# Optimization experiments

Measured on AMD Instinct MI355X. Metric: run time of the kernel, lower is better.

The kernel has to match this reference:

```python
import jax, jax.numpy as jnp
import numpy as np

VEC_DIM = 64
RANK = 2


def setup_inputs() -> dict:
    key = jax.random.key(0)
    kg, km, kp = jax.random.split(key, 3)
    grid = jax.random.normal(kg, (193, 193, VEC_DIM), dtype=jnp.float32)
    # nn.init.uniform_(M.weight, -0.5, 0.5)
    M_weight = jax.random.uniform(km, (VEC_DIM, VEC_DIM), minval=-0.5, maxval=0.5, dtype=jnp.float32)
    # nn.init.uniform_(P, -0.1, 0.1)
    P = jax.random.uniform(kp, (VEC_DIM, VEC_DIM), minval=-0.1, maxval=0.1, dtype=jnp.float32)
    return {"grid": grid, "M_weight": M_weight, "P": P}


def reference(grid, M_weight, P):
    H, W, m = grid.shape
    # periods1[i,j] = periods2[i,j] = i*m + j + 2
    periods = (jnp.arange(m, dtype=jnp.float32)[:, None] * m
               + jnp.arange(m, dtype=jnp.float32)[None, :] + 2.0)  # [m, m]

    # ---- window extraction: linear mode (step=1), rank_mode='drop', rank_op='avg' ----
    nH = H - RANK + 1
    nW = W - RANK + 1
    win_sum = jax.lax.reduce_window(grid, 0.0, jax.lax.add,
                                    (RANK, RANK, 1), (1, 1, 1), 'VALID')  # [nH, nW, m]
    x_win = (win_sum / float(RANK * RANK)).reshape(nH * nW, m)  # [B, m]

    # ---- map through M (nn.Linear, no bias): y = x @ W^T ----
    x = x_win @ M_weight.T  # [B, m]

    # ---- phi_table gather: phi[k1,k2] = cos(2*pi*k1/periods) * cos(2*pi*k2/periods) ----
    two_pi = jnp.float32(2.0 * np.pi)
    k1s = jnp.arange(nH, dtype=jnp.float32)
    k2s = jnp.arange(nW, dtype=jnp.float32)
    cos1 = jnp.cos(two_pi * k1s[:, None, None] / periods)  # [nH, m, m]
    cos2 = jnp.cos(two_pi * k2s[:, None, None] / periods)  # [nW, m, m]
    phi = (cos1[:, None, :, :] * cos2[None, :, :, :]).reshape(nH * nW, m, m)  # [B, m, m]

    # ---- Nk = einsum('bj,ij,bij->bi', x, P, phi) ----
    Nk = jnp.einsum('bj,ij,bij->bi', x, P, phi)  # [B, m]
    return Nk
```

## Files before the change

kernel.cpp:

```cpp
#include <hip/hip_runtime.h>
#include <math.h>

#define NH 192
#define NW 192
#define Wt 193
#define TG 24
#define NTILE (TG*TG)
#define TILE_SZ 4096
#define NMAIN 768
#define CHUNK 48

__device__ __forceinline__ float cos_revr(float num, float rcpden) {
    float rev = num * rcpden;
    rev = __builtin_amdgcn_fractf(rev);
    return __builtin_amdgcn_cosf(rev);
}

__global__ __launch_bounds__(256) void k_prep(const float* __restrict__ grid,
                                              const float* __restrict__ Mw,
                                              float* __restrict__ xt) {
    __shared__ float Ms[64 * 64];
    __shared__ float win[64 * 68];
    int bb = blockIdx.x;
    int t = threadIdx.x;
    int k1g = bb % TG, k2g = bb / TG;

    #pragma unroll
    for (int r = 0; r < 4; ++r) {
        int e = r * 256 + t;
        ((float4*)Ms)[e] = ((const float4*)Mw)[e];
    }

    {
        int c = t & 63, pq = t >> 6;
        const float* gb = grid + ((size_t)(k1g * 8) * Wt + k2g * 8) * 64;
        #pragma unroll
        for (int r = 0; r < 16; ++r) {
            int p = pq * 16 + r;
            int l1 = p >> 3, l2 = p & 7;
            const float* g0 = gb + ((size_t)l1 * Wt + l2) * 64;
            float s = g0[c] + g0[64 + c] + g0[Wt * 64 + c] + g0[Wt * 64 + 64 + c];
            win[p * 68 + c] = 0.25f * s;
        }
    }
    __syncthreads();

    int p = t & 63, jq = t >> 6;
    float4 wv[16];
    #pragma unroll
    for (int q = 0; q < 16; ++q) wv[q] = *(const float4*)&win[p * 68 + 4 * q];

    float* xb = xt + (size_t)(k1g * TG + k2g) * TILE_SZ;
    #pragma unroll
    for (int r = 0; r < 16; ++r) {
        int j = jq * 16 + r;
        float acc = 0.f;
        #pragma unroll
        for (int q = 0; q < 16; ++q) {
            float4 mv = *(const float4*)&Ms[j * 64 + 4 * q];
            acc += wv[q].x * mv.x + wv[q].y * mv.y + wv[q].z * mv.z + wv[q].w * mv.w;
        }
        xb[(size_t)j * 64 + p] = acc;
    }
}

__global__ __launch_bounds__(256, 3) void k_main(const float* __restrict__ xt,
                                                 const float* __restrict__ P,
                                                 float* __restrict__ out) {
    __shared__ float xls[CHUNK * 68];
    __shared__ float pp[4096];
    int bx = blockIdx.x;
    int k1 = bx >> 2;
    int c  = bx & 3;
    int k2s = c * CHUNK;
    int t = threadIdx.x;
    int lane = t & 63;
    int w = __builtin_amdgcn_readfirstlane(t >> 6);
    int jb = w * 16;

    {
        const float4* P4 = (const float4*)P;
        #pragma unroll
        for (int s = 0; s < 4; ++s) {
            int e = s * 256 + t;
            float4 v = P4[e];
            int i = e >> 4, j0 = (e & 15) * 4;
            pp[(j0 + 0) * 64 + i] = v.x;
            pp[(j0 + 1) * 64 + i] = v.y;
            pp[(j0 + 2) * 64 + i] = v.z;
            pp[(j0 + 3) * 64 + i] = v.w;
        }
    }
    {
        int prow = k1 & 7;
        const float4* xt4 = (const float4*)xt
                          + (size_t)((k1 >> 3) * TG + c * 6) * (TILE_SZ / 4);
        #pragma unroll
        for (int s = 0; s < 3; ++s) {
            int f = s * 256 + t;
            int j = f / 12, u = f - 12 * j;
            int tc = u >> 1, h = u & 1;
            float4 v = xt4[tc * 1024 + j * 16 + prow * 2 + h];
            int k2l = tc * 8 + h * 4;
            xls[(k2l + 0) * 68 + j] = v.x;
            xls[(k2l + 1) * 68 + j] = v.y;
            xls[(k2l + 2) * 68 + j] = v.z;
            xls[(k2l + 3) * 68 + j] = v.w;
        }
    }
    __syncthreads();

    float A[16], c1v[16], ce[16], co[16];
    #pragma unroll
    for (int jl = 0; jl < 16; ++jl) {
        float T  = (float)(lane * 64 + jb + jl + 2);
        float rT = __builtin_amdgcn_rcpf(T);
        A[jl]   = 2.0f * cos_revr(1.0f, rT);
        c1v[jl] = cos_revr((float)k1, rT) * pp[(jb + jl) * 64 + lane];
    }
    __syncthreads();

    float* part = pp;
    for (int sub = 0; sub < 3; ++sub) {
        int k2a = k2s + sub * 16;
        #pragma unroll
        for (int jl = 0; jl < 16; ++jl) {
            float T  = (float)(lane * 64 + jb + jl + 2);
            float rT = __builtin_amdgcn_rcpf(T);
            ce[jl] = cos_revr((float)k2a, rT);
            co[jl] = cos_revr((float)(k2a - 1), rT);
        }
        #pragma unroll
        for (int nn = 0; nn < 8; ++nn) {
            {
                const float4* xq = (const float4*)&xls[(sub * 16 + 2 * nn) * 68 + jb];
                float4 q0 = xq[0], q1 = xq[1], q2 = xq[2], q3 = xq[3];
                float xs[16] = {q0.x, q0.y, q0.z, q0.w, q1.x, q1.y, q1.z, q1.w,
                                q2.x, q2.y, q2.z, q2.w, q3.x, q3.y, q3.z, q3.w};
                float psum = 0.f;
                #pragma unroll
                for (int jl = 0; jl < 16; ++jl) {
                    psum   = fmaf(xs[jl] * c1v[jl], ce[jl], psum);
                    co[jl] = fmaf(A[jl], ce[jl], -co[jl]);
                }
                part[(w * 16 + 2 * nn) * 64 + lane] = psum;
            }
            {
                const float4* xq = (const float4*)&xls[(sub * 16 + 2 * nn + 1) * 68 + jb];
                float4 q0 = xq[0], q1 = xq[1], q2 = xq[2], q3 = xq[3];
                float xs[16] = {q0.x, q0.y, q0.z, q0.w, q1.x, q1.y, q1.z, q1.w,
                                q2.x, q2.y, q2.z, q2.w, q3.x, q3.y, q3.z, q3.w};
                float psum = 0.f;
                #pragma unroll
                for (int jl = 0; jl < 16; ++jl) {
                    psum   = fmaf(xs[jl] * c1v[jl], co[jl], psum);
                    ce[jl] = fmaf(A[jl], co[jl], -ce[jl]);
                }
                part[(w * 16 + 2 * nn + 1) * 64 + lane] = psum;
            }
        }
        __syncthreads();
        #pragma unroll
        for (int s = 0; s < 4; ++s) {
            int e = s * 256 + t;
            float r = part[e] + part[1024 + e] + part[2048 + e] + part[3072 + e];
            out[((size_t)k1 * NW + (k2a + (e >> 6))) * 64 + (e & 63)] = r;
        }
        __syncthreads();
    }
}

extern "C" void kernel_launch(void* const* d_in, const int* in_sizes, int n_in,
                              void* d_out, int out_size, void* d_ws, size_t ws_size,
                              hipStream_t stream) {
    const float* grid = (const float*)d_in[0];
    const float* Mw   = (const float*)d_in[1];
    const float* P    = (const float*)d_in[2];
    float* out = (float*)d_out;

    float* xt = (float*)d_ws;

    k_prep<<<NTILE, 256, 0, stream>>>(grid, Mw, xt);
    k_main<<<NMAIN, 256, 0, stream>>>(xt, P, out);
}
```

Baseline: 95.41 us.

## Fuse window-average and M projection into main kernel, drop workspace round trip

```diff
diff --git a/kernel.cpp b/kernel.cpp
--- a/kernel.cpp
+++ b/kernel.cpp
@@ -1,12 +1,8 @@
 #include <hip/hip_runtime.h>
 #include <math.h>
 
-#define NH 192
 #define NW 192
 #define Wt 193
-#define TG 24
-#define NTILE (TG*TG)
-#define TILE_SZ 4096
 #define NMAIN 768
 #define CHUNK 48
 
@@ -16,67 +12,61 @@
     return __builtin_amdgcn_cosf(rev);
 }
 
-__global__ __launch_bounds__(256) void k_prep(const float* __restrict__ grid,
-                                              const float* __restrict__ Mw,
-                                              float* __restrict__ xt) {
-    __shared__ float Ms[64 * 64];
-    __shared__ float win[64 * 68];
-    int bb = blockIdx.x;
+__global__ __launch_bounds__(256, 3) void k_fused(const float* __restrict__ grid,
+                                                  const float* __restrict__ Mw,
+                                                  const float* __restrict__ P,
+                                                  float* __restrict__ out) {
+    __shared__ float bufA[4096];
+    __shared__ float bufB[4096];
+    __shared__ float xls[CHUNK * 68];
+
+    int bx = blockIdx.x;
+    int k1  = bx >> 2;
+    int k2s = (bx & 3) * CHUNK;
     int t = threadIdx.x;
-    int k1g = bb % TG, k2g = bb / TG;
+    int lane = t & 63;
+    int w = __builtin_amdgcn_readfirstlane(t >> 6);
+    int jb = w * 16;
 
     #pragma unroll
     for (int r = 0; r < 4; ++r) {
         int e = r * 256 + t;
-        ((float4*)Ms)[e] = ((const float4*)Mw)[e];
+        ((float4*)bufB)[e] = ((const float4*)Mw)[e];
     }
-
     {
-        int c = t & 63, pq = t >> 6;
-        const float* gb = grid + ((size_t)(k1g * 8) * Wt + k2g * 8) * 64;
+        int c = t & 63;
+        const float* gb  = grid + ((size_t)k1 * Wt + k2s) * 64 + c;
+        const float* gb1 = gb + (size_t)Wt * 64;
         #pragma unroll
-        for (int r = 0; r < 16; ++r) {
-            int p = pq * 16 + r;
-            int l1 = p >> 3, l2 = p & 7;
-            const float* g0 = gb + ((size_t)l1 * Wt + l2) * 64;
-            float s = g0[c] + g0[64 + c] + g0[Wt * 64 + c] + g0[Wt * 64 + 64 + c];
-            win[p * 68 + c] = 0.25f * s;
+        for (int r = 0; r < 12; ++r) {
+            int p = w * 12 + r;
+            float s = gb[p * 64] + gb[(p + 1) * 64]
+                    + gb1[p * 64] + gb1[(p + 1) * 64];
+            bufA[p * 68 + c] = 0.25f * s;
         }
     }
     __syncthreads();
 
-    int p = t & 63, jq = t >> 6;
-    float4 wv[16];
-    #pragma unroll
-    for (int q = 0; q < 16; ++q) wv[q] = *(const float4*)&win[p * 68 + 4 * q];
-
-    float* xb = xt + (size_t)(k1g * TG + k2g) * TILE_SZ;
-    #pragma unroll
-    for (int r = 0; r < 16; ++r) {
-        int j = jq * 16 + r;
-        float acc = 0.f;
+    if (lane < 48) {
+        int p = lane;
+        float4 wv[16];
         #pragma unroll
-        for (int q = 0; q < 16; ++q) {
-            float4 mv = *(const float4*)&Ms[j * 64 + 4 * q];
-            acc += wv[q].x * mv.x + wv[q].y * mv.y + wv[q].z * mv.z + wv[q].w * mv.w;
+        for (int q = 0; q < 16; ++q) wv[q] = *(const float4*)&bufA[p * 68 + 4 * q];
+        #pragma unroll
+        for (int r = 0; r < 16; ++r) {
+            int j = jb + r;
+            const float4* mrow = (const float4*)&bufB[j * 64];
+            float acc = 0.f;
+            #pragma unroll
+            for (int q = 0; q < 16; ++q) {
+                float4 mv = mrow[q];
+                acc += wv[q].x * mv.x + wv[q].y * mv.y
+                     + wv[q].z * mv.z + wv[q].w * mv.w;
+            }
+            xls[p * 68 + j] = acc;
         }
-        xb[(size_t)j * 64 + p] = acc;
     }
-}
-
-__global__ __launch_bounds__(256, 3) void k_main(const float* __restrict__ xt,
-                                                 const float* __restrict__ P,
-                                                 float* __restrict__ out) {
-    __shared__ float xls[CHUNK * 68];
-    __shared__ float pp[4096];
-    int bx = blockIdx.x;
-    int k1 = bx >> 2;
-    int c  = bx & 3;
-    int k2s = c * CHUNK;
-    int t = threadIdx.x;
-    int lane = t & 63;
-    int w = __builtin_amdgcn_readfirstlane(t >> 6);
-    int jb = w * 16;
+    __syncthreads();
 
     {
         const float4* P4 = (const float4*)P;
@@ -85,27 +75,10 @@
             int e = s * 256 + t;
             float4 v = P4[e];
             int i = e >> 4, j0 = (e & 15) * 4;
-            pp[(j0 + 0) * 64 + i] = v.x;
-            pp[(j0 + 1) * 64 + i] = v.y;
-            pp[(j0 + 2) * 64 + i] = v.z;
-            pp[(j0 + 3) * 64 + i] = v.w;
-        }
-    }
-    {
-        int prow = k1 & 7;
-        const float4* xt4 = (const float4*)xt
-                          + (size_t)((k1 >> 3) * TG + c * 6) * (TILE_SZ / 4);
-        #pragma unroll
-        for (int s = 0; s < 3; ++s) {
-            int f = s * 256 + t;
-            int j = f / 12, u = f - 12 * j;
-            int tc = u >> 1, h = u & 1;
-            float4 v = xt4[tc * 1024 + j * 16 + prow * 2 + h];
-            int k2l = tc * 8 + h * 4;
-            xls[(k2l + 0) * 68 + j] = v.x;
-            xls[(k2l + 1) * 68 + j] = v.y;
-            xls[(k2l + 2) * 68 + j] = v.z;
-            xls[(k2l + 3) * 68 + j] = v.w;
+            bufA[(j0 + 0) * 64 + i] = v.x;
+            bufA[(j0 + 1) * 64 + i] = v.y;
+            bufA[(j0 + 2) * 64 + i] = v.z;
+            bufA[(j0 + 3) * 64 + i] = v.w;
         }
     }
     __syncthreads();
@@ -116,11 +89,10 @@
         float T  = (float)(lane * 64 + jb + jl + 2);
         float rT = __builtin_amdgcn_rcpf(T);
         A[jl]   = 2.0f * cos_revr(1.0f, rT);
-        c1v[jl] = cos_revr((float)k1, rT) * pp[(jb + jl) * 64 + lane];
+        c1v[jl] = cos_revr((float)k1, rT) * bufA[(jb + jl) * 64 + lane];
     }
-    __syncthreads();
 
-    float* part = pp;
+    float* part = bufB;
     for (int sub = 0; sub < 3; ++sub) {
         int k2a = k2s + sub * 16;
         #pragma unroll
@@ -177,9 +149,7 @@
     const float* Mw   = (const float*)d_in[1];
     const float* P    = (const float*)d_in[2];
     float* out = (float*)d_out;
+    (void)d_ws; (void)ws_size;
 
-    float* xt = (float*)d_ws;
-
-    k_prep<<<NTILE, 256, 0, stream>>>(grid, Mw, xt);
-    k_main<<<NMAIN, 256, 0, stream>>>(xt, P, out);
+    k_fused<<<NMAIN, 256, 0, stream>>>(grid, Mw, P, out);
 }
```

New measurement: 95.33 us. About the same (-0.1%).
